# Kernel tuning notes

Measured on AMD Instinct MI355X. Metric: run time of the kernel, lower is better.

The kernel has to match this reference:

```python
import jax, jax.numpy as jnp
import numpy as np

B, N, HN, HE, H = 8, 128, 256, 128, 8
DH = HN // H
P = N * (N - 1) // 2


def _ln(x, g, b, eps=1e-5):
    m = jnp.mean(x, axis=-1, keepdims=True)
    v = jnp.mean((x - m) ** 2, axis=-1, keepdims=True)
    return (x - m) * jax.lax.rsqrt(v + eps) * g + b


def setup_inputs() -> dict:
    key = jax.random.key(0)
    ks = jax.random.split(key, 16)
    i1, i2 = np.triu_indices(N, k=1)  # all unordered pairs, P = N(N-1)/2
    s = lambda fan: 1.0 / np.sqrt(fan)
    return {
        "node_feat": jax.random.normal(ks[0], (B, N, HN), jnp.float32),
        "edge_feat": jax.random.normal(ks[1], (B, P, HE), jnp.float32),
        "x_idx1": jnp.asarray(i1, jnp.int32),
        "x_idx2": jnp.asarray(i2, jnp.int32),
        "mask_valid": jax.random.bernoulli(ks[2], 0.9, (B, P)).astype(jnp.float32),
        "Wqkv": jax.random.normal(ks[3], (HN, 3 * HN), jnp.float32) * s(HN),
        "bqkv": jnp.zeros((3 * HN,), jnp.float32),
        "Wev": jax.random.normal(ks[4], (HE, HN), jnp.float32) * s(HE),
        "bev": jnp.zeros((HN,), jnp.float32),
        "Wea": jax.random.normal(ks[5], (HE, H), jnp.float32) * s(HE),
        "bea": jnp.zeros((H,), jnp.float32),
        "Wo": jax.random.normal(ks[6], (2 * HN, HN), jnp.float32) * s(2 * HN),
        "bo": jnp.zeros((HN,), jnp.float32),
        "Wsk": jax.random.normal(ks[7], (HN, 2 * HN), jnp.float32) * s(HN),
        "bsk": jnp.zeros((2 * HN,), jnp.float32),
        "gn": jnp.ones((HN,), jnp.float32),
        "bn": jnp.zeros((HN,), jnp.float32),
        "ge": jnp.ones((HE,), jnp.float32),
        "be": jnp.zeros((HE,), jnp.float32),
    }


def reference(node_feat, edge_feat, x_idx1, x_idx2, mask_valid,
              Wqkv, bqkv, Wev, bev, Wea, bea, Wo, bo, Wsk, bsk,
              gn, bn, ge, be):
    n_in = _ln(node_feat, gn, bn)                      # [B,N,HN]
    e_in = _ln(edge_feat, ge, be)                      # [B,P,HE]
    q, k, v = jnp.split(n_in @ Wqkv + bqkv, 3, axis=-1)
    to_h = lambda t: t.reshape(B, -1, H, DH).transpose(0, 2, 1, 3)
    q, k, v = to_h(q), to_h(k), to_h(v)                # [B,H,N,DH]
    e_val = to_h(e_in @ Wev + bev)                     # [B,H,P,DH]
    e_adj = (e_in @ Wea + bea).transpose(0, 2, 1)      # [B,H,P]

    scale = DH ** -0.5
    logits = jnp.einsum('bhqd,bhkd->bhqk', q, k) * scale  # [B,H,N,N]
    # per-pair logits; torch stacks [qk, edge_adj] then sums -> just add
    l_node1 = logits[:, :, x_idx1, x_idx2] + e_adj     # node i1 attends to i2
    l_node2 = logits[:, :, x_idx2, x_idx1] + e_adj     # node i2 attends to i1
    v_node1 = e_val + v[:, :, x_idx2]                  # value node i1 receives
    v_node2 = e_val + v[:, :, x_idx1]

    # group the 2P directed edges by destination node (= torch cat+sort+reshape)
    cat_idx = jnp.concatenate([x_idx1, x_idx2])        # [2P]
    order = jnp.argsort(cat_idx)                       # stable sort
    gl = jnp.concatenate([l_node1, l_node2], axis=2)[:, :, order].reshape(B, H, N, N - 1)
    gv = jnp.concatenate([v_node1, v_node2], axis=2)[:, :, order].reshape(B, H, N, N - 1, DH)
    gm = jnp.concatenate([mask_valid, mask_valid], axis=1)[:, order].reshape(B, N, N - 1)[:, None]  # [B,1,N,N-1]

    gl = jnp.where(gm == 0.0, -9e15, gl)
    probs = jax.nn.softmax(gl, axis=3)
    probs = probs * jnp.any(gm != 0.0, axis=3, keepdims=True).astype(probs.dtype)
    attn = jnp.einsum('bhnk,bhnkd->bhnd', probs, gv)   # [B,H,N,DH]
    attn = attn.transpose(0, 2, 1, 3).reshape(B, N, HN)

    comb = jax.nn.gelu(jnp.concatenate([n_in, attn], axis=-1) @ Wo + bo, approximate=False)
    val, gate = jnp.split(comb @ Wsk + bsk, 2, axis=-1)
    g = jax.nn.sigmoid(gate)
    return node_feat * (1.0 - g) + val * g
```

## Files before the change

kernel.cpp:

```cpp
#include <hip/hip_runtime.h>
#include <hip/hip_bf16.h>
#include <math.h>

#define BB 8
#define NN 128
#define HN 256
#define HE 128
#define NH 8
#define DH 32
#define PP 8128
#define BP (BB*PP)

typedef __hip_bfloat16 bf16;
typedef __hip_bfloat162 bf162;
typedef __attribute__((ext_vector_type(8))) short bf16x8;
typedef __attribute__((ext_vector_type(4))) float f32x4;

__device__ __forceinline__ float bf2f(bf16 x){ return __bfloat162float(x); }
__device__ __forceinline__ float bfraw2f(short u){
  return __uint_as_float(((unsigned)(unsigned short)u) << 16);
}

__device__ __forceinline__ float wave_sum(float v){
  #pragma unroll
  for (int off=32; off>=1; off>>=1) v += __shfl_xor(v, off, 64);
  return v;
}
__device__ __forceinline__ float g16_sum(float v){
  #pragma unroll
  for (int off=8; off>=1; off>>=1) v += __shfl_xor(v, off, 16);
  return v;
}

__device__ __forceinline__ int pair_idx(int a, int c){
  int i = a < c ? a : c;
  int j = a < c ? c : a;
  return ((i*(255 - i))>>1) + (j - i - 1);
}

#define C_NODE 0LL
#define C_MASK 262144LL
#define C_WQKV 327168LL
#define C_BQKV 523776LL
#define C_WEV  524544LL
#define C_BEV  557312LL
#define C_WEA  557568LL
#define C_BEA  558592LL
#define C_WO   558600LL
#define C_BO   689672LL
#define C_WSK  689928LL
#define C_BSK  821000LL
#define C_GN   821512LL
#define C_BN   821768LL
#define C_GE   822024LL
#define C_BE   822152LL
#define IOFF   822400LL
#define TOT8   102785
#define CONVBLKS 402
#define I_NIN  0LL
#define I_Q    262144LL
#define I_K    524288LL
#define I_V    786432LL
#define I_ATTN 1048576LL
#define I_COMB 1310720LL
#define I_EA2  1572864LL
#define I_XG   2093056LL
#define I_WT   14577664LL
#define I_WOB  14594048LL
#define I_WSKB 14659584LL
#define I_FLG  14725120LL

struct SrcPtrs { const void* p[16]; };

__global__ __launch_bounds__(256) void k_convert(SrcPtrs sp, float* __restrict__ dst,
                                                 int* __restrict__ flags,
                                                 const unsigned short* __restrict__ nodeRaw,
                                                 const void* __restrict__ rawWev,
                                                 bf16* __restrict__ Wt,
                                                 const void* __restrict__ rawWo,
                                                 const void* __restrict__ rawWsk,
                                                 bf16* __restrict__ WoB,
                                                 bf16* __restrict__ WskB)
{
  __shared__ int sbad;
  if (threadIdx.x == 0) sbad = 0;
  __syncthreads();
  {
    int bad = 0;
    for (int i = threadIdx.x; i < 1024; i += 256){
      unsigned e = (nodeRaw[i] >> 7) & 0xFFu;
      if (e >= 194u) bad = 1;
    }
    if (bad) sbad = 1;
  }
  __syncthreads();
  const int f32 = sbad;
  if (blockIdx.x == 0 && threadIdx.x == 0) flags[0] = f32;

  if (blockIdx.x >= CONVBLKS + 128){
    int o = (blockIdx.x - (CONVBLKS + 128))*256 + threadIdx.x;
    const void* src = (o < 16384) ? rawWo : rawWsk;
    bf16* dw = (o < 16384) ? WoB : WskB;
    int lo = (o < 16384) ? o : o - 16384;
    if (f32){
      const float4* s4 = (const float4*)src;
      float4 a0 = s4[2*lo], a1 = s4[2*lo+1];
      union { float4 f; bf16 h[8]; } cv;
      cv.h[0]=__float2bfloat16(a0.x); cv.h[1]=__float2bfloat16(a0.y);
      cv.h[2]=__float2bfloat16(a0.z); cv.h[3]=__float2bfloat16(a0.w);
      cv.h[4]=__float2bfloat16(a1.x); cv.h[5]=__float2bfloat16(a1.y);
      cv.h[6]=__float2bfloat16(a1.z); cv.h[7]=__float2bfloat16(a1.w);
      *reinterpret_cast<float4*>(dw + lo*8) = cv.f;
    } else {
      *reinterpret_cast<float4*>(dw + lo*8) = ((const float4*)src)[lo];
    }
    return;
  }

  if (blockIdx.x >= CONVBLKS){
    int idx = (blockIdx.x - CONVBLKS)*256 + threadIdx.x;
    float v = f32 ? ((const float*)rawWev)[idx]
                  : bfraw2f(((const short*)rawWev)[idx]);
    Wt[(idx & 255)*128 + (idx >> 8)] = __float2bfloat16(v);
    return;
  }

  int o = blockIdx.x*256 + threadIdx.x;
  if (o >= TOT8) return;
  const int cum[17] = {0,32768,40896,65472,65568,69664,69696,69824,69825,
                       86209,86241,102625,102689,102721,102753,102769,102785};
  int s = 0;
  #pragma unroll
  for (int i = 1; i <= 15; i++) if (o >= cum[i]) s = i;
  const int li = o - cum[s];
  float4 r0, r1;
  if (f32){
    const float4* src = (const float4*)sp.p[s];
    r0 = src[2*li]; r1 = src[2*li+1];
  } else {
    union { float4 f; unsigned short u[8]; } cv;
    cv.f = ((const float4*)sp.p[s])[li];
    r0.x = __uint_as_float((unsigned)cv.u[0] << 16);
    r0.y = __uint_as_float((unsigned)cv.u[1] << 16);
    r0.z = __uint_as_float((unsigned)cv.u[2] << 16);
    r0.w = __uint_as_float((unsigned)cv.u[3] << 16);
    r1.x = __uint_as_float((unsigned)cv.u[4] << 16);
    r1.y = __uint_as_float((unsigned)cv.u[5] << 16);
    r1.z = __uint_as_float((unsigned)cv.u[6] << 16);
    r1.w = __uint_as_float((unsigned)cv.u[7] << 16);
  }
  float4* d = (float4*)(dst + (long long)cum[s]*8);
  d[2*li]   = r0;
  d[2*li+1] = r1;
}

__global__ __launch_bounds__(256) void k1_node_ln_qkv(
    const float* __restrict__ cnode, const float* __restrict__ cWqkv,
    const float* __restrict__ cbqkv, const float* __restrict__ cgn, const float* __restrict__ cbn,
    float* __restrict__ nin_ws, float* __restrict__ q_ws, float* __restrict__ k_ws,
    float* __restrict__ v_ws)
{
  __shared__ float xln[4][HN];
  const int t = threadIdx.x, wv = t>>6, lane = t&63;
  const int cb = blockIdx.x % 3;
  const int g0 = (blockIdx.x / 3) * 4;
  {
    int g = g0 + wv;
    float x[4];
    #pragma unroll
    for (int i=0;i<4;i++) x[i] = cnode[g*HN + lane + 64*i];
    float s = x[0]+x[1]+x[2]+x[3];
    s = wave_sum(s);
    float m = s * (1.0f/HN);
    float q = 0.f;
    #pragma unroll
    for (int i=0;i<4;i++){ float d = x[i]-m; q += d*d; }
    q = wave_sum(q);
    float rstd = rsqrtf(fmaxf(q*(1.0f/HN), 0.f) + 1e-5f);
    #pragma unroll
    for (int i=0;i<4;i++){
      int c = lane + 64*i;
      float y = (x[i]-m)*rstd*cgn[c] + cbn[c];
      xln[wv][c] = y;
      if (cb == 0) nin_ws[g*HN + c] = y;
    }
  }
  __syncthreads();
  const int col = cb*256 + t;
  float acc[4];
  {
    float bb = cbqkv[col];
    #pragma unroll
    for (int r=0;r<4;r++) acc[r] = bb;
  }
  for (int k=0;k<HN;k+=4){
    float4 xv[4];
    #pragma unroll
    for (int r=0;r<4;r++) xv[r] = *reinterpret_cast<const float4*>(&xln[r][k]);
    #pragma unroll
    for (int kk=0;kk<4;kk++){
      float w = cWqkv[(k+kk)*768 + col];
      #pragma unroll
      for (int r=0;r<4;r++) acc[r] = fmaf((&xv[r].x)[kk], w, acc[r]);
    }
  }
  if (cb == 2){
    #pragma unroll
    for (int r=0;r<4;r++) v_ws[(long)(g0+r)*HN + t] = acc[r];
  } else {
    float* dstp = (cb == 0) ? q_ws : k_ws;
    const int h = t>>5, d = t&31;
    #pragma unroll
    for (int r=0;r<4;r++){
      int g = g0 + r;
      int b = g>>7, n = g&127;
      dstp[((b*NH + h)*NN + n)*DH + d] = acc[r];
    }
  }
}

__global__ __launch_bounds__(256) void k2a_edge_ln(
    const void* __restrict__ edge_raw, const float* __restrict__ cWea,
    const float* __restrict__ cbea, const float* __restrict__ cge,
    const float* __restrict__ cbe, const float* __restrict__ cmask,
    bf16* __restrict__ xg, float* __restrict__ ea2, const int* __restrict__ flags)
{
  __shared__ float xlnS[16][136];
  __shared__ float part[128];
  const int t = threadIdx.x;
  const int R0 = blockIdx.x*16;
  const int b = R0 / PP;
  const int p0 = R0 - b*PP;
  const int f32 = flags[0];
  {
    int r = t>>4, sub = t&15;
    long base = (long)(R0 + r)*HE + sub*8;
    float x[8];
    if (f32){
      const float* cef = (const float*)edge_raw + base;
      float4 a0 = *reinterpret_cast<const float4*>(cef);
      float4 a1 = *reinterpret_cast<const float4*>(cef + 4);
      x[0]=a0.x; x[1]=a0.y; x[2]=a0.z; x[3]=a0.w;
      x[4]=a1.x; x[5]=a1.y; x[6]=a1.z; x[7]=a1.w;
    } else {
      union { float4 f; short u[8]; } cv;
      cv.f = *reinterpret_cast<const float4*>((const bf16*)edge_raw + base);
      #pragma unroll
      for (int i=0;i<8;i++) x[i] = bfraw2f(cv.u[i]);
    }
    float s = 0.f;
    #pragma unroll
    for (int i=0;i<8;i++) s += x[i];
    s = g16_sum(s);
    float m = s*(1.0f/HE);
    float q = 0.f;
    #pragma unroll
    for (int i=0;i<8;i++){ float dd = x[i]-m; q += dd*dd; }
    q = g16_sum(q);
    float rstd = rsqrtf(fmaxf(q*(1.0f/HE), 0.f) + 1e-5f);
    #pragma unroll
    for (int i=0;i<8;i++){
      int c = sub*8 + i;
      xlnS[r][c] = (x[i]-m)*rstd*cge[c] + cbe[c];
    }
  }
  __syncthreads();
  {
    int r = t>>4, c0 = (t&15)*8;
    union { float4 f; bf16 h[8]; } o;
    #pragma unroll
    for (int i=0;i<8;i++) o.h[i] = __float2bfloat16(xlnS[r][c0+i]);
    *reinterpret_cast<float4*>(xg + (long)(R0 + r)*HE + c0) = o.f;
  }
  {
    const int c = t & 7, r = (t>>3) & 15, half = t>>7;
    const int pid = r*8 + c;
    float s = half ? 0.0f : cbea[c];
    const int k0 = half*64;
    #pragma unroll 8
    for (int k=k0; k<k0+64; k++) s = fmaf(xlnS[r][k], cWea[k*NH + c], s);
    if (half){ part[pid] = s; }
    __syncthreads();
    if (!half){
      s += part[pid];
      int p = p0 + r;
      float mk = cmask[b*PP + p];
      ea2[((long)b*PP + p)*8 + c] = (mk != 0.0f) ? s : -9e15f;
    }
  }
}

__global__ __launch_bounds__(256, 4) void k3_attn(
    const float* __restrict__ q_ws,
    const float* __restrict__ k_ws,
    const float* __restrict__ v_ws,
    const bf16* __restrict__ xg,
    const float* __restrict__ ea2,
    const bf16* __restrict__ Wt,
    const float* __restrict__ cbev,
    float* __restrict__ attn)
{
  __shared__ __align__(16) bf16  xgS[128][128];
  __shared__ __align__(16) float sS[8][128];
  const int t = threadIdx.x;
  const int bid = blockIdx.x;
  const int swz = (bid & 7)*128 + (bid >> 3);
  const int n = swz & 127, b = swz >> 7;
  const int h = t >> 5, ln = t & 31;

  float4 qv[8];
  const float* qb = q_ws + (((long)b*NH + h)*NN + n)*DH;
  #pragma unroll
  for (int d4=0; d4<8; d4++) qv[d4] = *reinterpret_cast<const float4*>(qb + d4*4);
  float eav[4];
  const float* eab = ea2 + (long)b*PP*8;
  #pragma unroll
  for (int j=0;j<4;j++){
    int m = ln + 32*j;
    int ms = (m == n) ? (m ^ 1) : m;
    eav[j] = eab[(long)pair_idx(n, ms)*8 + h];
  }
  const bf16* xgb = xg + (long)b*PP*HE;
  const int rowb = t >> 4, seg = t & 15;
  float4 xr[8];
  #pragma unroll
  for (int it=0; it<8; ++it){
    int row = it*16 + rowb;
    int ms = (row == n) ? (row ^ 1) : row;
    int pr = pair_idx(n, ms);
    xr[it] = *reinterpret_cast<const float4*>(xgb + (long)pr*HE + seg*8);
  }

  const float scale = 0.17677669529663687f;
  const float* kb = k_ws + ((long)b*NH + h)*NN*DH;
  float l[4];
  float mx = -INFINITY;
  int valid = 0;
  #pragma unroll
  for (int j=0;j<4;j++){
    int m = ln + 32*j;
    const float* kr = kb + m*DH;
    float dot = 0.f;
    #pragma unroll
    for (int d4=0; d4<8; d4++){
      float4 kv = *reinterpret_cast<const float4*>(kr + d4*4);
      dot = fmaf(qv[d4].x, kv.x, dot);
      dot = fmaf(qv[d4].y, kv.y, dot);
      dot = fmaf(qv[d4].z, kv.z, dot);
      dot = fmaf(qv[d4].w, kv.w, dot);
    }
    bool self = (m == n);
    l[j] = self ? -INFINITY : fmaf(dot, scale, eav[j]);
    if (!self && eav[j] > -8.9e15f) valid = 1;
    mx = fmaxf(mx, l[j]);
  }
  #pragma unroll
  for (int off=16; off>=1; off>>=1) mx = fmaxf(mx, __shfl_xor(mx, off, 32));
  float e[4], s = 0.f;
  #pragma unroll
  for (int j=0;j<4;j++){ e[j] = __expf(l[j]-mx); s += e[j]; }
  float av = valid ? 1.f : 0.f;
  #pragma unroll
  for (int off=16; off>=1; off>>=1){
    s  += __shfl_xor(s,  off, 32);
    av += __shfl_xor(av, off, 32);
  }
  float inv = (av > 0.f) ? (1.0f/s) : 0.f;
  float pj0 = e[0]*inv, pj1 = e[1]*inv, pj2 = e[2]*inv, pj3 = e[3]*inv;

  #pragma unroll
  for (int it=0; it<8; ++it){
    int row = it*16 + rowb;
    *reinterpret_cast<float4*>(&xgS[row][seg*8]) = xr[it];
  }
  __syncthreads();

  const float* vb = v_ws + (long)b*NN*HN + h*DH + ln;
  float S0=0.f,S1=0.f,S2=0.f,S3=0.f,T=0.f;
  #pragma unroll
  for (int j=0;j<4;j++){
    float pcur = (j==0) ? pj0 : (j==1) ? pj1 : (j==2) ? pj2 : pj3;
    #pragma unroll 2
    for (int mm=0; mm<32; mm+=4){
      #pragma unroll
      for (int i=0;i<4;i++){
        int m = j*32 + mm + i;
        float pm = __shfl(pcur, mm + i, 32);
        short4 xv = *reinterpret_cast<const short4*>(&xgS[m][ln*4]);
        S0 = fmaf(pm, bfraw2f(xv.x), S0);
        S1 = fmaf(pm, bfraw2f(xv.y), S1);
        S2 = fmaf(pm, bfraw2f(xv.z), S2);
        S3 = fmaf(pm, bfraw2f(xv.w), S3);
        T  = fmaf(pm, vb[m*HN], T);
      }
    }
  }
  {
    float4 sv; sv.x=S0; sv.y=S1; sv.z=S2; sv.w=S3;
    *reinterpret_cast<float4*>(&sS[h][ln*4]) = sv;
  }
  __syncthreads();

  float acc = T + ((av > 0.f) ? cbev[h*DH + ln] : 0.f);
  const bf16* wr = Wt + (h*DH + ln)*HE;
  #pragma unroll 4
  for (int k0=0;k0<128;k0+=8){
    float4 sa = *reinterpret_cast<const float4*>(&sS[h][k0]);
    float4 sb = *reinterpret_cast<const float4*>(&sS[h][k0+4]);
    bf16x8 wv = *reinterpret_cast<const bf16x8*>(wr + k0);
    acc = fmaf(sa.x, bfraw2f(wv[0]), acc);
    acc = fmaf(sa.y, bfraw2f(wv[1]), acc);
    acc = fmaf(sa.z, bfraw2f(wv[2]), acc);
    acc = fmaf(sa.w, bfraw2f(wv[3]), acc);
    acc = fmaf(sb.x, bfraw2f(wv[4]), acc);
    acc = fmaf(sb.y, bfraw2f(wv[5]), acc);
    acc = fmaf(sb.z, bfraw2f(wv[6]), acc);
    acc = fmaf(sb.w, bfraw2f(wv[7]), acc);
  }
  attn[((long)b*NN + n)*HN + h*DH + ln] = acc;
}

__global__ __launch_bounds__(256) void k4_wo_gelu(
    const float* __restrict__ nin_ws, const float* __restrict__ attn,
    const bf16* __restrict__ WoB, const float* __restrict__ cbo,
    float* __restrict__ comb)
{
  __shared__ float xc[4][512];
  __shared__ float ps[3][4][64];
  const int t = threadIdx.x;
  const int g0 = (blockIdx.x >> 2) * 4;
  const int cq = blockIdx.x & 3;
  {
    int r = t>>6, c0 = (t&63)*8;
    const float* src = (c0 < 256) ? (nin_ws + (long)(g0+r)*HN + c0)
                                  : (attn + (long)(g0+r)*HN + (c0-256));
    float4 a0 = *reinterpret_cast<const float4*>(src);
    float4 a1 = *reinterpret_cast<const float4*>(src+4);
    *reinterpret_cast<float4*>(&xc[r][c0]) = a0;
    *reinterpret_cast<float4*>(&xc[r][c0+4]) = a1;
  }
  __syncthreads();
  const int cidx = t & 63, ks = t >> 6;
  const int col = cq*64 + cidx;
  float acc[4] = {0.f,0.f,0.f,0.f};
  const int k0 = ks*128;
  #pragma unroll 4
  for (int k=k0; k<k0+128; k++){
    float w = bf2f(WoB[k*HN + col]);
    #pragma unroll
    for (int r=0;r<4;r++) acc[r] = fmaf(xc[r][k], w, acc[r]);
  }
  if (ks){
    #pragma unroll
    for (int r=0;r<4;r++) ps[ks-1][r][cidx] = acc[r];
  }
  __syncthreads();
  if (!ks){
    float bb = cbo[col];
    #pragma unroll
    for (int r=0;r<4;r++){
      float x = acc[r] + bb + ps[0][r][cidx] + ps[1][r][cidx] + ps[2][r][cidx];
      comb[(long)(g0+r)*HN + col] = 0.5f*x*(1.0f + erff(x*0.7071067811865475f));
    }
  }
}

__global__ __launch_bounds__(256) void k5_sk_gate(
    const float* __restrict__ comb, const float* __restrict__ cnode,
    const bf16* __restrict__ WskB, const float* __restrict__ cbsk,
    void* __restrict__ out, const int* __restrict__ flags)
{
  __shared__ float xc[4][HN];
  __shared__ float psv[3][4][64];
  __shared__ float psg[3][4][64];
  const int t = threadIdx.x;
  const int g0 = (blockIdx.x >> 2) * 4;
  const int cq = blockIdx.x & 3;
  {
    int r = t>>6, c0 = (t&63)*4;
    *reinterpret_cast<float4*>(&xc[r][c0]) =
        *reinterpret_cast<const float4*>(comb + (long)(g0+r)*HN + c0);
  }
  __syncthreads();
  const int cidx = t & 63, ks = t >> 6;
  const int col = cq*64 + cidx;
  float av[4] = {0.f,0.f,0.f,0.f}, ag[4] = {0.f,0.f,0.f,0.f};
  const int k0 = ks*64;
  #pragma unroll 4
  for (int k=k0; k<k0+64; k++){
    float wv = bf2f(WskB[k*512 + col]);
    float wg = bf2f(WskB[k*512 + col + 256]);
    #pragma unroll
    for (int r=0;r<4;r++){
      float xr = xc[r][k];
      av[r] = fmaf(xr, wv, av[r]);
      ag[r] = fmaf(xr, wg, ag[r]);
    }
  }
  if (ks){
    #pragma unroll
    for (int r=0;r<4;r++){ psv[ks-1][r][cidx] = av[r]; psg[ks-1][r][cidx] = ag[r]; }
  }
  __syncthreads();
  if (!ks){
    const int f32 = flags[0];
    float bv = cbsk[col], bg = cbsk[col+256];
    #pragma unroll
    for (int r=0;r<4;r++){
      float v = av[r] + bv + psv[0][r][cidx] + psv[1][r][cidx] + psv[2][r][cidx];
      float g = ag[r] + bg + psg[0][r][cidx] + psg[1][r][cidx] + psg[2][r][cidx];
      float gg = 1.0f/(1.0f + __expf(-g));
      float nf = cnode[(long)(g0+r)*HN + col];
      float res = nf*(1.0f - gg) + v*gg;
      if (f32) ((float*)out)[(long)(g0+r)*HN + col] = res;
      else ((bf16*)out)[(long)(g0+r)*HN + col] = __float2bfloat16(res);
    }
  }
}

extern "C" void kernel_launch(void* const* d_in, const int* in_sizes, int n_inputs,
                              void* d_out, int out_size, void* d_ws, size_t ws_size,
                              hipStream_t stream)
{
  float* ws = (float*)d_ws;
  float* c_node = ws + C_NODE;
  float* c_mask = ws + C_MASK;
  float* c_Wqkv = ws + C_WQKV;
  float* c_bqkv = ws + C_BQKV;
  float* c_bev  = ws + C_BEV;
  float* c_Wea  = ws + C_WEA;
  float* c_bea  = ws + C_BEA;
  float* c_bo   = ws + C_BO;
  float* c_bsk  = ws + C_BSK;
  float* c_gn   = ws + C_GN;
  float* c_bn   = ws + C_BN;
  float* c_ge   = ws + C_GE;
  float* c_be   = ws + C_BE;
  float* base   = ws + IOFF;
  float* nin_ws  = base + I_NIN;
  float* q_ws    = base + I_Q;
  float* k_ws    = base + I_K;
  float* v_ws    = base + I_V;
  float* attn_ws = base + I_ATTN;
  float* comb_ws = base + I_COMB;
  float* ea2_ws  = base + I_EA2;
  bf16*  xg_ws   = (bf16*)(base + I_XG);
  bf16*  wt_ws   = (bf16*)(base + I_WT);
  bf16*  wob_ws  = (bf16*)(base + I_WOB);
  bf16*  wskb_ws = (bf16*)(base + I_WSKB);
  int*   flags   = (int*)(base + I_FLG);

  SrcPtrs sp;
  sp.p[0]  = d_in[0];
  sp.p[1]  = d_in[4];
  sp.p[2]  = d_in[5];
  sp.p[3]  = d_in[6];
  sp.p[4]  = d_in[7];
  sp.p[5]  = d_in[8];
  sp.p[6]  = d_in[9];
  sp.p[7]  = d_in[10];
  sp.p[8]  = d_in[11];
  sp.p[9]  = d_in[12];
  sp.p[10] = d_in[13];
  sp.p[11] = d_in[14];
  sp.p[12] = d_in[15];
  sp.p[13] = d_in[16];
  sp.p[14] = d_in[17];
  sp.p[15] = d_in[18];

  k_convert<<<CONVBLKS + 256, 256, 0, stream>>>(sp, ws, flags,
                                                (const unsigned short*)d_in[0],
                                                d_in[7], wt_ws,
                                                d_in[11], d_in[13],
                                                wob_ws, wskb_ws);
  k1_node_ln_qkv<<<768, 256, 0, stream>>>(c_node, c_Wqkv, c_bqkv, c_gn, c_bn,
                                          nin_ws, q_ws, k_ws, v_ws);
  k2a_edge_ln<<<BP/16, 256, 0, stream>>>(d_in[1], c_Wea, c_bea, c_ge, c_be, c_mask,
                                         xg_ws, ea2_ws, flags);
  k3_attn<<<BB*NN, 256, 0, stream>>>(q_ws, k_ws, v_ws, xg_ws, ea2_ws, wt_ws, c_bev,
                                     attn_ws);
  k4_wo_gelu<<<1024, 256, 0, stream>>>(nin_ws, attn_ws, wob_ws, c_bo, comb_ws);
  k5_sk_gate<<<1024, 256, 0, stream>>>(comb_ws, c_node, wskb_ws, c_bsk, d_out, flags);
}
```

Before: 198.0 us.

## Fuse attention, Wo+GELU and skip-gate projections into one per-node kernel

Merges the attention kernel with the Wo/GELU and Wsk/sigmoid-gate kernels, so each block (one node) keeps its attention output and combined vector in shared memory instead of writing them to global workspace. Wo and Wsk are pre-transposed in the convert kernel so each thread reads a contiguous weight row with 16-byte bf16x8 loads. The edge-LN store to shared memory is also vectorised. In exchange, each block now streams the full Wo and Wsk matrices per node without reuse across rows, where the old kernels reused each weight over 4 rows, so weight traffic per output rises and leans on cache.

```diff
diff --git a/kernel.cpp b/kernel.cpp
--- a/kernel.cpp
+++ b/kernel.cpp
@@ -12,9 +12,7 @@
 #define BP (BB*PP)
 
 typedef __hip_bfloat16 bf16;
-typedef __hip_bfloat162 bf162;
 typedef __attribute__((ext_vector_type(8))) short bf16x8;
-typedef __attribute__((ext_vector_type(4))) float f32x4;
 
 __device__ __forceinline__ float bf2f(bf16 x){ return __bfloat162float(x); }
 __device__ __forceinline__ float bfraw2f(short u){
@@ -61,13 +59,11 @@
 #define I_Q    262144LL
 #define I_K    524288LL
 #define I_V    786432LL
-#define I_ATTN 1048576LL
-#define I_COMB 1310720LL
 #define I_EA2  1572864LL
 #define I_XG   2093056LL
 #define I_WT   14577664LL
-#define I_WOB  14594048LL
-#define I_WSKB 14659584LL
+#define I_WOT  14594048LL
+#define I_WSKT 14659584LL
 #define I_FLG  14725120LL
 
 struct SrcPtrs { const void* p[16]; };
@@ -79,8 +75,8 @@
                                                  bf16* __restrict__ Wt,
                                                  const void* __restrict__ rawWo,
                                                  const void* __restrict__ rawWsk,
-                                                 bf16* __restrict__ WoB,
-                                                 bf16* __restrict__ WskB)
+                                                 bf16* __restrict__ WoT,
+                                                 bf16* __restrict__ WskT)
 {
   __shared__ int sbad;
   if (threadIdx.x == 0) sbad = 0;
@@ -99,20 +95,34 @@
 
   if (blockIdx.x >= CONVBLKS + 128){
     int o = (blockIdx.x - (CONVBLKS + 128))*256 + threadIdx.x;
-    const void* src = (o < 16384) ? rawWo : rawWsk;
-    bf16* dw = (o < 16384) ? WoB : WskB;
-    int lo = (o < 16384) ? o : o - 16384;
-    if (f32){
-      const float4* s4 = (const float4*)src;
-      float4 a0 = s4[2*lo], a1 = s4[2*lo+1];
-      union { float4 f; bf16 h[8]; } cv;
-      cv.h[0]=__float2bfloat16(a0.x); cv.h[1]=__float2bfloat16(a0.y);
-      cv.h[2]=__float2bfloat16(a0.z); cv.h[3]=__float2bfloat16(a0.w);
-      cv.h[4]=__float2bfloat16(a1.x); cv.h[5]=__float2bfloat16(a1.y);
-      cv.h[6]=__float2bfloat16(a1.z); cv.h[7]=__float2bfloat16(a1.w);
-      *reinterpret_cast<float4*>(dw + lo*8) = cv.f;
+    union { float4 f; bf16 h[8]; } cv;
+    if (o < 16384){
+      int outb = o*8;
+      int n = outb >> 9, k0 = outb & 511;
+      if (f32){
+        const float* src = (const float*)rawWo;
+        #pragma unroll
+        for (int i=0;i<8;i++) cv.h[i] = __float2bfloat16(src[(long)(k0+i)*HN + n]);
+      } else {
+        const bf16* src = (const bf16*)rawWo;
+        #pragma unroll
+        for (int i=0;i<8;i++) cv.h[i] = src[(long)(k0+i)*HN + n];
+      }
+      *reinterpret_cast<float4*>(WoT + outb) = cv.f;
     } else {
-      *reinterpret_cast<float4*>(dw + lo*8) = ((const float4*)src)[lo];
+      int lo = o - 16384;
+      int outb = lo*8;
+      int c = outb >> 8, k0 = outb & 255;
+      if (f32){
+        const float* src = (const float*)rawWsk;
+        #pragma unroll
+        for (int i=0;i<8;i++) cv.h[i] = __float2bfloat16(src[(long)(k0+i)*512 + c]);
+      } else {
+        const bf16* src = (const bf16*)rawWsk;
+        #pragma unroll
+        for (int i=0;i<8;i++) cv.h[i] = src[(long)(k0+i)*512 + c];
+      }
+      *reinterpret_cast<float4*>(WskT + outb) = cv.f;
     }
     return;
   }
@@ -258,11 +268,16 @@
     for (int i=0;i<8;i++){ float dd = x[i]-m; q += dd*dd; }
     q = g16_sum(q);
     float rstd = rsqrtf(fmaxf(q*(1.0f/HE), 0.f) + 1e-5f);
+    float y[8];
     #pragma unroll
     for (int i=0;i<8;i++){
       int c = sub*8 + i;
-      xlnS[r][c] = (x[i]-m)*rstd*cge[c] + cbe[c];
-    }
+      y[i] = (x[i]-m)*rstd*cge[c] + cbe[c];
+    }
+    float4 y0; y0.x=y[0]; y0.y=y[1]; y0.z=y[2]; y0.w=y[3];
+    float4 y1; y1.x=y[4]; y1.y=y[5]; y1.z=y[6]; y1.w=y[7];
+    *reinterpret_cast<float4*>(&xlnS[r][sub*8])     = y0;
+    *reinterpret_cast<float4*>(&xlnS[r][sub*8 + 4]) = y1;
   }
   __syncthreads();
   {
@@ -290,7 +305,7 @@
   }
 }
 
-__global__ __launch_bounds__(256, 4) void k3_attn(
+__global__ __launch_bounds__(256, 4) void k345(
     const float* __restrict__ q_ws,
     const float* __restrict__ k_ws,
     const float* __restrict__ v_ws,
@@ -298,14 +313,23 @@
     const float* __restrict__ ea2,
     const bf16* __restrict__ Wt,
     const float* __restrict__ cbev,
-    float* __restrict__ attn)
+    const float* __restrict__ nin_ws,
+    const bf16* __restrict__ WoT,
+    const float* __restrict__ cbo,
+    const bf16* __restrict__ WskT,
+    const float* __restrict__ cbsk,
+    const float* __restrict__ cnode,
+    void* __restrict__ out, const int* __restrict__ flags)
 {
   __shared__ __align__(16) bf16  xgS[128][128];
   __shared__ __align__(16) float sS[8][128];
+  float* xc    = (float*)xgS;
+  float* combS = xc + 512;
   const int t = threadIdx.x;
   const int bid = blockIdx.x;
   const int swz = (bid & 7)*128 + (bid >> 3);
   const int n = swz & 127, b = swz >> 7;
+  const int g = b*NN + n;
   const int h = t >> 5, ln = t & 31;
 
   float4 qv[8];
@@ -401,8 +425,9 @@
   }
   __syncthreads();
 
-  float acc = T + ((av > 0.f) ? cbev[h*DH + ln] : 0.f);
-  const bf16* wr = Wt + (h*DH + ln)*HE;
+  float nin_v = nin_ws[(long)g*HN + t];
+  float acc = T + ((av > 0.f) ? cbev[t] : 0.f);
+  const bf16* wr = Wt + t*HE;
   #pragma unroll 4
   for (int k0=0;k0<128;k0+=8){
     float4 sa = *reinterpret_cast<const float4*>(&sS[h][k0]);
@@ -417,105 +442,62 @@
     acc = fmaf(sb.z, bfraw2f(wv[6]), acc);
     acc = fmaf(sb.w, bfraw2f(wv[7]), acc);
   }
-  attn[((long)b*NN + n)*HN + h*DH + ln] = acc;
-}
-
-__global__ __launch_bounds__(256) void k4_wo_gelu(
-    const float* __restrict__ nin_ws, const float* __restrict__ attn,
-    const bf16* __restrict__ WoB, const float* __restrict__ cbo,
-    float* __restrict__ comb)
-{
-  __shared__ float xc[4][512];
-  __shared__ float ps[3][4][64];
-  const int t = threadIdx.x;
-  const int g0 = (blockIdx.x >> 2) * 4;
-  const int cq = blockIdx.x & 3;
-  {
-    int r = t>>6, c0 = (t&63)*8;
-    const float* src = (c0 < 256) ? (nin_ws + (long)(g0+r)*HN + c0)
-                                  : (attn + (long)(g0+r)*HN + (c0-256));
-    float4 a0 = *reinterpret_cast<const float4*>(src);
-    float4 a1 = *reinterpret_cast<const float4*>(src+4);
-    *reinterpret_cast<float4*>(&xc[r][c0]) = a0;
-    *reinterpret_cast<float4*>(&xc[r][c0+4]) = a1;
-  }
-  __syncthreads();
-  const int cidx = t & 63, ks = t >> 6;
-  const int col = cq*64 + cidx;
-  float acc[4] = {0.f,0.f,0.f,0.f};
-  const int k0 = ks*128;
+  xc[t]       = nin_v;
+  xc[256 + t] = acc;
+  __syncthreads();
+
+  float co = cbo[t];
+  const bf16* worow = WoT + t*512;
+  #pragma unroll 8
+  for (int k0=0;k0<512;k0+=8){
+    bf16x8 w8 = *reinterpret_cast<const bf16x8*>(worow + k0);
+    float4 xa = *reinterpret_cast<const float4*>(&xc[k0]);
+    float4 xb = *reinterpret_cast<const float4*>(&xc[k0+4]);
+    co = fmaf(xa.x, bfraw2f(w8[0]), co);
+    co = fmaf(xa.y, bfraw2f(w8[1]), co);
+    co = fmaf(xa.z, bfraw2f(w8[2]), co);
+    co = fmaf(xa.w, bfraw2f(w8[3]), co);
+    co = fmaf(xb.x, bfraw2f(w8[4]), co);
+    co = fmaf(xb.y, bfraw2f(w8[5]), co);
+    co = fmaf(xb.z, bfraw2f(w8[6]), co);
+    co = fmaf(xb.w, bfraw2f(w8[7]), co);
+  }
+  co = 0.5f*co*(1.0f + erff(co*0.7071067811865475f));
+  combS[t] = co;
+  __syncthreads();
+
+  float av5 = cbsk[t], ag5 = cbsk[t+256];
+  const bf16* wvrow = WskT + t*256;
+  const bf16* wgrow = WskT + (t+256)*256;
   #pragma unroll 4
-  for (int k=k0; k<k0+128; k++){
-    float w = bf2f(WoB[k*HN + col]);
-    #pragma unroll
-    for (int r=0;r<4;r++) acc[r] = fmaf(xc[r][k], w, acc[r]);
-  }
-  if (ks){
-    #pragma unroll
-    for (int r=0;r<4;r++) ps[ks-1][r][cidx] = acc[r];
-  }
-  __syncthreads();
-  if (!ks){
-    float bb = cbo[col];
-    #pragma unroll
-    for (int r=0;r<4;r++){
-      float x = acc[r] + bb + ps[0][r][cidx] + ps[1][r][cidx] + ps[2][r][cidx];
-      comb[(long)(g0+r)*HN + col] = 0.5f*x*(1.0f + erff(x*0.7071067811865475f));
-    }
-  }
-}
-
-__global__ __launch_bounds__(256) void k5_sk_gate(
-    const float* __restrict__ comb, const float* __restrict__ cnode,
-    const bf16* __restrict__ WskB, const float* __restrict__ cbsk,
-    void* __restrict__ out, const int* __restrict__ flags)
-{
-  __shared__ float xc[4][HN];
-  __shared__ float psv[3][4][64];
-  __shared__ float psg[3][4][64];
-  const int t = threadIdx.x;
-  const int g0 = (blockIdx.x >> 2) * 4;
-  const int cq = blockIdx.x & 3;
-  {
-    int r = t>>6, c0 = (t&63)*4;
-    *reinterpret_cast<float4*>(&xc[r][c0]) =
-        *reinterpret_cast<const float4*>(comb + (long)(g0+r)*HN + c0);
-  }
-  __syncthreads();
-  const int cidx = t & 63, ks = t >> 6;
-  const int col = cq*64 + cidx;
-  float av[4] = {0.f,0.f,0.f,0.f}, ag[4] = {0.f,0.f,0.f,0.f};
-  const int k0 = ks*64;
-  #pragma unroll 4
-  for (int k=k0; k<k0+64; k++){
-    float wv = bf2f(WskB[k*512 + col]);
-    float wg = bf2f(WskB[k*512 + col + 256]);
-    #pragma unroll
-    for (int r=0;r<4;r++){
-      float xr = xc[r][k];
-      av[r] = fmaf(xr, wv, av[r]);
-      ag[r] = fmaf(xr, wg, ag[r]);
-    }
-  }
-  if (ks){
-    #pragma unroll
-    for (int r=0;r<4;r++){ psv[ks-1][r][cidx] = av[r]; psg[ks-1][r][cidx] = ag[r]; }
-  }
-  __syncthreads();
-  if (!ks){
-    const int f32 = flags[0];
-    float bv = cbsk[col], bg = cbsk[col+256];
-    #pragma unroll
-    for (int r=0;r<4;r++){
-      float v = av[r] + bv + psv[0][r][cidx] + psv[1][r][cidx] + psv[2][r][cidx];
-      float g = ag[r] + bg + psg[0][r][cidx] + psg[1][r][cidx] + psg[2][r][cidx];
-      float gg = 1.0f/(1.0f + __expf(-g));
-      float nf = cnode[(long)(g0+r)*HN + col];
-      float res = nf*(1.0f - gg) + v*gg;
-      if (f32) ((float*)out)[(long)(g0+r)*HN + col] = res;
-      else ((bf16*)out)[(long)(g0+r)*HN + col] = __float2bfloat16(res);
-    }
-  }
+  for (int k0=0;k0<256;k0+=8){
+    bf16x8 wv8 = *reinterpret_cast<const bf16x8*>(wvrow + k0);
+    bf16x8 wg8 = *reinterpret_cast<const bf16x8*>(wgrow + k0);
+    float4 ca = *reinterpret_cast<const float4*>(&combS[k0]);
+    float4 cb2 = *reinterpret_cast<const float4*>(&combS[k0+4]);
+    av5 = fmaf(ca.x,  bfraw2f(wv8[0]), av5);
+    av5 = fmaf(ca.y,  bfraw2f(wv8[1]), av5);
+    av5 = fmaf(ca.z,  bfraw2f(wv8[2]), av5);
+    av5 = fmaf(ca.w,  bfraw2f(wv8[3]), av5);
+    av5 = fmaf(cb2.x, bfraw2f(wv8[4]), av5);
+    av5 = fmaf(cb2.y, bfraw2f(wv8[5]), av5);
+    av5 = fmaf(cb2.z, bfraw2f(wv8[6]), av5);
+    av5 = fmaf(cb2.w, bfraw2f(wv8[7]), av5);
+    ag5 = fmaf(ca.x,  bfraw2f(wg8[0]), ag5);
+    ag5 = fmaf(ca.y,  bfraw2f(wg8[1]), ag5);
+    ag5 = fmaf(ca.z,  bfraw2f(wg8[2]), ag5);
+    ag5 = fmaf(ca.w,  bfraw2f(wg8[3]), ag5);
+    ag5 = fmaf(cb2.x, bfraw2f(wg8[4]), ag5);
+    ag5 = fmaf(cb2.y, bfraw2f(wg8[5]), ag5);
+    ag5 = fmaf(cb2.z, bfraw2f(wg8[6]), ag5);
+    ag5 = fmaf(cb2.w, bfraw2f(wg8[7]), ag5);
+  }
+  float gg = 1.0f/(1.0f + __expf(-ag5));
+  long idx = (long)g*HN + t;
+  float nf = cnode[idx];
+  float res = nf*(1.0f - gg) + av5*gg;
+  if (flags[0]) ((float*)out)[idx] = res;
+  else ((bf16*)out)[idx] = __float2bfloat16(res);
 }
 
 extern "C" void kernel_launch(void* const* d_in, const int* in_sizes, int n_inputs,
@@ -541,13 +523,11 @@
   float* q_ws    = base + I_Q;
   float* k_ws    = base + I_K;
   float* v_ws    = base + I_V;
-  float* attn_ws = base + I_ATTN;
-  float* comb_ws = base + I_COMB;
   float* ea2_ws  = base + I_EA2;
   bf16*  xg_ws   = (bf16*)(base + I_XG);
   bf16*  wt_ws   = (bf16*)(base + I_WT);
-  bf16*  wob_ws  = (bf16*)(base + I_WOB);
-  bf16*  wskb_ws = (bf16*)(base + I_WSKB);
+  bf16*  wot_ws  = (bf16*)(base + I_WOT);
+  bf16*  wskt_ws = (bf16*)(base + I_WSKT);
   int*   flags   = (int*)(base + I_FLG);
 
   SrcPtrs sp;
@@ -572,13 +552,12 @@
                                                 (const unsigned short*)d_in[0],
                                                 d_in[7], wt_ws,
                                                 d_in[11], d_in[13],
-                                                wob_ws, wskb_ws);
+                                                wot_ws, wskt_ws);
   k1_node_ln_qkv<<<768, 256, 0, stream>>>(c_node, c_Wqkv, c_bqkv, c_gn, c_bn,
                                           nin_ws, q_ws, k_ws, v_ws);
   k2a_edge_ln<<<BP/16, 256, 0, stream>>>(d_in[1], c_Wea, c_bea, c_ge, c_be, c_mask,
                                          xg_ws, ea2_ws, flags);
-  k3_attn<<<BB*NN, 256, 0, stream>>>(q_ws, k_ws, v_ws, xg_ws, ea2_ws, wt_ws, c_bev,
-                                     attn_ws);
-  k4_wo_gelu<<<1024, 256, 0, stream>>>(nin_ws, attn_ws, wob_ws, c_bo, comb_ws);
-  k5_sk_gate<<<1024, 256, 0, stream>>>(comb_ws, c_node, wskb_ws, c_bsk, d_out, flags);
-}
+  k345<<<BB*NN, 256, 0, stream>>>(q_ws, k_ws, v_ws, xg_ws, ea2_ws, wt_ws, c_bev,
+                                  nin_ws, wot_ws, c_bo, wskt_ws, c_bsk,
+                                  c_node, d_out, flags);
+}
```

Result: slower. 256.1 us (+29.3%).
